# Kernel optimization log

Measured on AMD Instinct MI355X. Metric: run time of the kernel, lower is better.

The kernel has to match this reference:

```python
import jax, jax.numpy as jnp
import numpy as np
from jax import lax

# Fixed LBP neighbor-difference filters: each of 8 filters is (neighbor - center)
_LBP_W = np.array([
    [[[0,0,1],[0,-1,0],[0,0,0]]],
    [[[0,0,0],[0,-1,1],[0,0,0]]],
    [[[0,0,0],[0,-1,0],[0,0,1]]],
    [[[0,0,0],[0,-1,0],[0,1,0]]],
    [[[0,0,0],[0,-1,0],[1,0,0]]],
    [[[0,0,0],[1,-1,0],[0,0,0]]],
    [[[1,0,0],[0,-1,0],[0,0,0]]],
    [[[0,1,0],[0,-1,0],[0,0,0]]],
], dtype=np.float32)  # [8,1,3,3] OIHW

_RGB2GRAY = np.array([0.299, 0.587, 0.114], dtype=np.float32)


def setup_inputs() -> dict:
    key = jax.random.key(0)
    img = jax.random.uniform(key, (16, 3, 1024, 1024), dtype=jnp.float32)
    lbp_weight = jnp.asarray(_LBP_W)                                   # [8,1,3,3]
    kernel_weight = jnp.asarray(2.0 ** np.arange(8, dtype=np.float32)  # 1,2,...,128
                                ).reshape(1, 8, 1, 1)
    return {"img": img, "lbp_weight": lbp_weight, "kernel_weight": kernel_weight}


def reference(img, lbp_weight, kernel_weight):
    # rgb2gray: [B,3,H,W] -> [B,1,H,W]
    gray = jnp.einsum("bchw,c->bhw", img, jnp.asarray(_RGB2GRAY))[:, None]
    # 3x3 LBP neighbor-difference conv, padding=1 (SAME)
    out = lax.conv_general_dilated(
        gray, lbp_weight, window_strides=(1, 1), padding=((1, 1), (1, 1)),
        dimension_numbers=("NCHW", "OIHW", "NCHW"))                    # [B,8,H,W]
    # threshold then weighted sum of bit-planes -> LBP code in [0,255]
    bits = jnp.where(out >= 0.0, 1.0, 0.0)
    lbp_img = jnp.sum(bits * kernel_weight, axis=1)                     # [B,H,W]
    # 256-bin histogram over ALL elements (matches torch.where counting loop)
    idx = lbp_img.astype(jnp.int32).reshape(-1)
    hist = jnp.zeros((1, 256), dtype=jnp.float32).at[0, idx].add(1.0)
    # standardize with unbiased std (torch.std default, ddof=1)
    mean = jnp.mean(hist, axis=1, keepdims=True)
    std = jnp.sqrt(jnp.sum((hist - mean) ** 2, axis=1, keepdims=True) / (256 - 1))
    return (hist - mean) / std
```

## Files before the change

kernel.cpp:

```cpp
#include <hip/hip_runtime.h>

#define NBATCH  16
#define NSTRIPS 16
#define SEGROWS 64
#define NSEGS   (1024 / SEGROWS)
#define NWAVES  (NBATCH * NSEGS * NSTRIPS)
#define NBLOCKS (NWAVES / 4)
#define NHIST   8

__device__ __forceinline__ float gray3(float r, float g, float b) {
    return (r * 0.299f + g * 0.587f) + b * 0.114f;
}

__global__ __launch_bounds__(256) void lbp_hist_kernel(
        const float* __restrict__ img, unsigned* __restrict__ g_hist) {
    __shared__ unsigned s_hist[4][256];
    const int tid  = threadIdx.x;
    const int wv   = tid >> 6;
    const int lane = tid & 63;
    #pragma unroll
    for (int i = 0; i < 4; ++i) s_hist[i][tid] = 0u;
    __syncthreads();

    const int w     = blockIdx.x * 4 + wv;
    const int strip = w & (NSTRIPS - 1);
    const int seg   = (w >> 4) & (NSEGS - 1);
    const int b     = w >> 8;
    const int wx    = strip << 6;
    const int x     = wx + lane;
    const int y0    = seg * SEGROWS;
    const int ylast = y0 + SEGROWS;

    const float* R = img + (size_t)b * 3145728u;
    const float* G = R + 1048576;
    const float* B = R + 2097152;

    const bool hL  = (lane == 0);
    const bool hR  = (lane == 63);
    const int  hx  = hL ? (wx - 1) : (wx + 64);
    const bool hOk = (hL || hR) && ((unsigned)hx < 1024u);

    auto issue = [&](int y, float& rr, float& gg, float& bb,
                     float& hr2, float& hg2, float& hb2) {
        rr = gg = bb = hr2 = hg2 = hb2 = 0.f;
        if ((unsigned)y < 1024u && y <= ylast) {
            const int o = y << 10;
            rr = R[o + x]; gg = G[o + x]; bb = B[o + x];
            if (hOk) { hr2 = R[o + hx]; hg2 = G[o + hx]; hb2 = B[o + hx]; }
        }
    };
    auto finish = [&](float rr, float gg, float bb, float hr2, float hg2, float hb2,
                      float& l, float& c, float& r) {
        const float cc = gray3(rr, gg, bb);
        const float hh = gray3(hr2, hg2, hb2);
        l = __shfl_up(cc, 1);
        r = __shfl_down(cc, 1);
        if (hL) l = hh;
        if (hR) r = hh;
        c = cc;
    };

    float r0l, r0c, r0r, r1l, r1c, r1r, r2l, r2c, r2r;
    float p1r, p1g, p1b, p1hr, p1hg, p1hb;
    float p2r, p2g, p2b, p2hr, p2hg, p2hb;
    float nr,  ng,  nb,  nhr,  nhg,  nhb;

    issue(y0 - 1, p1r, p1g, p1b, p1hr, p1hg, p1hb);
    finish(p1r, p1g, p1b, p1hr, p1hg, p1hb, r0l, r0c, r0r);
    issue(y0,     p1r, p1g, p1b, p1hr, p1hg, p1hb);
    finish(p1r, p1g, p1b, p1hr, p1hg, p1hb, r1l, r1c, r1r);
    issue(y0 + 1, p1r, p1g, p1b, p1hr, p1hg, p1hb);
    issue(y0 + 2, p2r, p2g, p2b, p2hr, p2hg, p2hb);

    unsigned cnt0 = 0u, cnt255 = 0u;

    #pragma unroll 4
    for (int y = y0; y < y0 + SEGROWS; ++y) {
        issue(y + 3, nr, ng, nb, nhr, nhg, nhb);
        finish(p1r, p1g, p1b, p1hr, p1hg, p1hb, r2l, r2c, r2r);

        const unsigned code =
            (r0r >= r1c ?   1u : 0u) |
            (r1r >= r1c ?   2u : 0u) |
            (r2r >= r1c ?   4u : 0u) |
            (r2c >= r1c ?   8u : 0u) |
            (r2l >= r1c ?  16u : 0u) |
            (r1l >= r1c ?  32u : 0u) |
            (r0l >= r1c ?  64u : 0u) |
            (r0c >= r1c ? 128u : 0u);

        cnt0   += (unsigned)__popcll(__ballot(code ==   0u));
        cnt255 += (unsigned)__popcll(__ballot(code == 255u));
        if ((code - 1u) < 254u)
            atomicAdd(&s_hist[wv][code], 1u);

        r0l = r1l; r0c = r1c; r0r = r1r;
        r1l = r2l; r1c = r2c; r1r = r2r;
        p1r = p2r; p1g = p2g; p1b = p2b; p1hr = p2hr; p1hg = p2hg; p1hb = p2hb;
        p2r = nr;  p2g = ng;  p2b = nb;  p2hr = nhr;  p2hg = nhg;  p2hb = nhb;
    }

    if (lane == 0) {
        atomicAdd(&s_hist[wv][0],   cnt0);
        atomicAdd(&s_hist[wv][255], cnt255);
    }
    __syncthreads();
    const unsigned total = s_hist[0][tid] + s_hist[1][tid] + s_hist[2][tid] + s_hist[3][tid];
    atomicAdd(&g_hist[((blockIdx.x & (NHIST - 1)) << 8) + tid], total);
}

__global__ __launch_bounds__(256) void lbp_finalize(
        const unsigned* __restrict__ g_hist, float* __restrict__ out) {
    __shared__ float red[256];
    const int i = threadIdx.x;
    unsigned hv = 0u;
    #pragma unroll
    for (int c = 0; c < NHIST; ++c) hv += g_hist[(c << 8) + i];
    const float h = (float)hv;
    red[i] = h;
    __syncthreads();
    #pragma unroll
    for (int s = 128; s > 0; s >>= 1) {
        if (i < s) red[i] += red[i + s];
        __syncthreads();
    }
    const float mean = red[0] * (1.0f / 256.0f);
    __syncthreads();
    const float d = h - mean;
    red[i] = d * d;
    __syncthreads();
    #pragma unroll
    for (int s = 128; s > 0; s >>= 1) {
        if (i < s) red[i] += red[i + s];
        __syncthreads();
    }
    const float stdv = sqrtf(red[0] * (1.0f / 255.0f));
    out[i] = d / stdv;
}

extern "C" void kernel_launch(void* const* d_in, const int* in_sizes, int n_in,
                              void* d_out, int out_size, void* d_ws, size_t ws_size,
                              hipStream_t stream) {
    const float* img = (const float*)d_in[0];
    unsigned* g_hist = (unsigned*)d_ws;
    float* out = (float*)d_out;

    hipMemsetAsync(g_hist, 0, NHIST * 256 * sizeof(unsigned), stream);
    lbp_hist_kernel<<<NBLOCKS, 256, 0, stream>>>(img, g_hist);
    lbp_finalize<<<1, 256, 0, stream>>>(g_hist, out);
}
```

Baseline: 283.2 us.

## Vectorize loads to float4 per lane and fuse finalize into last block

Each lane now handles four adjacent columns using float4 loads, so a wave covers 256 columns. The segment height is halved to keep enough waves in flight, and launch bounds request two blocks per CU. The separate finalize kernel is folded into the histogram kernel: the last block to finish, found through an atomic counter, performs the standardization. This cuts the number of load instructions and one kernel launch, at the cost of more registers per thread and a threadfence/atomic handshake at the end of every block.

```diff
diff --git a/kernel.cpp b/kernel.cpp
--- a/kernel.cpp
+++ b/kernel.cpp
@@ -1,10 +1,11 @@
 #include <hip/hip_runtime.h>
 
 #define NBATCH  16
-#define NSTRIPS 16
-#define SEGROWS 64
+#define COLS_W  256
+#define NSTRIPS (1024 / COLS_W)
+#define SEGROWS 32
 #define NSEGS   (1024 / SEGROWS)
-#define NWAVES  (NBATCH * NSEGS * NSTRIPS)
+#define NWAVES  (NBATCH * NSTRIPS * NSEGS)
 #define NBLOCKS (NWAVES / 4)
 #define NHIST   8
 
@@ -12,9 +13,12 @@
     return (r * 0.299f + g * 0.587f) + b * 0.114f;
 }
 
-__global__ __launch_bounds__(256) void lbp_hist_kernel(
-        const float* __restrict__ img, unsigned* __restrict__ g_hist) {
+__global__ __launch_bounds__(256, 2) void lbp_hist_kernel(
+        const float* __restrict__ img, unsigned* __restrict__ g_hist,
+        float* __restrict__ out) {
     __shared__ unsigned s_hist[4][256];
+    __shared__ float red[256];
+    __shared__ int s_last;
     const int tid  = threadIdx.x;
     const int wv   = tid >> 6;
     const int lane = tid & 63;
@@ -24,10 +28,10 @@
 
     const int w     = blockIdx.x * 4 + wv;
     const int strip = w & (NSTRIPS - 1);
-    const int seg   = (w >> 4) & (NSEGS - 1);
-    const int b     = w >> 8;
-    const int wx    = strip << 6;
-    const int x     = wx + lane;
+    const int seg   = (w >> 2) & (NSEGS - 1);
+    const int b     = w >> 7;
+    const int wx    = strip * COLS_W;
+    const int x     = wx + 4 * lane;
     const int y0    = seg * SEGROWS;
     const int ylast = y0 + SEGROWS;
 
@@ -37,38 +41,43 @@
 
     const bool hL  = (lane == 0);
     const bool hR  = (lane == 63);
-    const int  hx  = hL ? (wx - 1) : (wx + 64);
+    const int  hx  = hL ? (wx - 1) : (wx + COLS_W);
     const bool hOk = (hL || hR) && ((unsigned)hx < 1024u);
 
-    auto issue = [&](int y, float& rr, float& gg, float& bb,
+    auto issue = [&](int y, float4& rr, float4& gg, float4& bb,
                      float& hr2, float& hg2, float& hb2) {
-        rr = gg = bb = hr2 = hg2 = hb2 = 0.f;
+        rr = gg = bb = make_float4(0.f, 0.f, 0.f, 0.f);
+        hr2 = hg2 = hb2 = 0.f;
         if ((unsigned)y < 1024u && y <= ylast) {
             const int o = y << 10;
-            rr = R[o + x]; gg = G[o + x]; bb = B[o + x];
+            rr = *(const float4*)(R + o + x);
+            gg = *(const float4*)(G + o + x);
+            bb = *(const float4*)(B + o + x);
             if (hOk) { hr2 = R[o + hx]; hg2 = G[o + hx]; hb2 = B[o + hx]; }
         }
     };
-    auto finish = [&](float rr, float gg, float bb, float hr2, float hg2, float hb2,
-                      float& l, float& c, float& r) {
-        const float cc = gray3(rr, gg, bb);
+    auto finish = [&](const float4& rr, const float4& gg, const float4& bb,
+                      float hr2, float hg2, float hb2, float* row) {
+        row[1] = gray3(rr.x, gg.x, bb.x);
+        row[2] = gray3(rr.y, gg.y, bb.y);
+        row[3] = gray3(rr.z, gg.z, bb.z);
+        row[4] = gray3(rr.w, gg.w, bb.w);
         const float hh = gray3(hr2, hg2, hb2);
-        l = __shfl_up(cc, 1);
-        r = __shfl_down(cc, 1);
-        if (hL) l = hh;
-        if (hR) r = hh;
-        c = cc;
+        const float lu = __shfl_up(row[4], 1);
+        const float rd = __shfl_down(row[1], 1);
+        row[0] = hL ? hh : lu;
+        row[5] = hR ? hh : rd;
     };
 
-    float r0l, r0c, r0r, r1l, r1c, r1r, r2l, r2c, r2r;
-    float p1r, p1g, p1b, p1hr, p1hg, p1hb;
-    float p2r, p2g, p2b, p2hr, p2hg, p2hb;
-    float nr,  ng,  nb,  nhr,  nhg,  nhb;
+    float r0[6], r1[6], r2[6];
+    float4 p1r, p1g, p1b;  float p1hr, p1hg, p1hb;
+    float4 p2r, p2g, p2b;  float p2hr, p2hg, p2hb;
+    float4 nr,  ng,  nb;   float nhr,  nhg,  nhb;
 
     issue(y0 - 1, p1r, p1g, p1b, p1hr, p1hg, p1hb);
-    finish(p1r, p1g, p1b, p1hr, p1hg, p1hb, r0l, r0c, r0r);
+    finish(p1r, p1g, p1b, p1hr, p1hg, p1hb, r0);
     issue(y0,     p1r, p1g, p1b, p1hr, p1hg, p1hb);
-    finish(p1r, p1g, p1b, p1hr, p1hg, p1hb, r1l, r1c, r1r);
+    finish(p1r, p1g, p1b, p1hr, p1hg, p1hb, r1);
     issue(y0 + 1, p1r, p1g, p1b, p1hr, p1hg, p1hb);
     issue(y0 + 2, p2r, p2g, p2b, p2hr, p2hg, p2hb);
 
@@ -77,25 +86,28 @@
     #pragma unroll 4
     for (int y = y0; y < y0 + SEGROWS; ++y) {
         issue(y + 3, nr, ng, nb, nhr, nhg, nhb);
-        finish(p1r, p1g, p1b, p1hr, p1hg, p1hb, r2l, r2c, r2r);
+        finish(p1r, p1g, p1b, p1hr, p1hg, p1hb, r2);
 
-        const unsigned code =
-            (r0r >= r1c ?   1u : 0u) |
-            (r1r >= r1c ?   2u : 0u) |
-            (r2r >= r1c ?   4u : 0u) |
-            (r2c >= r1c ?   8u : 0u) |
-            (r2l >= r1c ?  16u : 0u) |
-            (r1l >= r1c ?  32u : 0u) |
-            (r0l >= r1c ?  64u : 0u) |
-            (r0c >= r1c ? 128u : 0u);
+        #pragma unroll
+        for (int k = 0; k < 4; ++k) {
+            const float c = r1[k + 1];
+            const unsigned code =
+                (r0[k + 2] >= c ?   1u : 0u) |
+                (r1[k + 2] >= c ?   2u : 0u) |
+                (r2[k + 2] >= c ?   4u : 0u) |
+                (r2[k + 1] >= c ?   8u : 0u) |
+                (r2[k]     >= c ?  16u : 0u) |
+                (r1[k]     >= c ?  32u : 0u) |
+                (r0[k]     >= c ?  64u : 0u) |
+                (r0[k + 1] >= c ? 128u : 0u);
+            cnt0   += (unsigned)__popcll(__ballot(code ==   0u));
+            cnt255 += (unsigned)__popcll(__ballot(code == 255u));
+            if ((code - 1u) < 254u)
+                atomicAdd(&s_hist[wv][code], 1u);
+        }
 
-        cnt0   += (unsigned)__popcll(__ballot(code ==   0u));
-        cnt255 += (unsigned)__popcll(__ballot(code == 255u));
-        if ((code - 1u) < 254u)
-            atomicAdd(&s_hist[wv][code], 1u);
-
-        r0l = r1l; r0c = r1c; r0r = r1r;
-        r1l = r2l; r1c = r2c; r1r = r2r;
+        #pragma unroll
+        for (int i = 0; i < 6; ++i) { r0[i] = r1[i]; r1[i] = r2[i]; }
         p1r = p2r; p1g = p2g; p1b = p2b; p1hr = p2hr; p1hg = p2hg; p1hb = p2hb;
         p2r = nr;  p2g = ng;  p2b = nb;  p2hr = nhr;  p2hg = nhg;  p2hb = nhb;
     }
@@ -107,35 +119,40 @@
     __syncthreads();
     const unsigned total = s_hist[0][tid] + s_hist[1][tid] + s_hist[2][tid] + s_hist[3][tid];
     atomicAdd(&g_hist[((blockIdx.x & (NHIST - 1)) << 8) + tid], total);
-}
 
-__global__ __launch_bounds__(256) void lbp_finalize(
-        const unsigned* __restrict__ g_hist, float* __restrict__ out) {
-    __shared__ float red[256];
-    const int i = threadIdx.x;
-    unsigned hv = 0u;
-    #pragma unroll
-    for (int c = 0; c < NHIST; ++c) hv += g_hist[(c << 8) + i];
-    const float h = (float)hv;
-    red[i] = h;
+    __threadfence();
+    if (tid == 0) {
+        const unsigned rank = atomicAdd(&g_hist[NHIST * 256], 1u);
+        s_last = (rank == NBLOCKS - 1) ? 1 : 0;
+    }
     __syncthreads();
-    #pragma unroll
-    for (int s = 128; s > 0; s >>= 1) {
-        if (i < s) red[i] += red[i + s];
+    if (s_last) {
+        __threadfence();
+        unsigned hv = 0u;
+        #pragma unroll
+        for (int c2 = 0; c2 < NHIST; ++c2)
+            hv += __hip_atomic_load(&g_hist[(c2 << 8) + tid],
+                                    __ATOMIC_RELAXED, __HIP_MEMORY_SCOPE_AGENT);
+        const float h = (float)hv;
+        red[tid] = h;
         __syncthreads();
+        #pragma unroll
+        for (int s = 128; s > 0; s >>= 1) {
+            if (tid < s) red[tid] += red[tid + s];
+            __syncthreads();
+        }
+        const float mean = red[0] * (1.0f / 256.0f);
+        __syncthreads();
+        const float d = h - mean;
+        red[tid] = d * d;
+        __syncthreads();
+        #pragma unroll
+        for (int s = 128; s > 0; s >>= 1) {
+            if (tid < s) red[tid] += red[tid + s];
+            __syncthreads();
+        }
+        out[tid] = d / sqrtf(red[0] * (1.0f / 255.0f));
     }
-    const float mean = red[0] * (1.0f / 256.0f);
-    __syncthreads();
-    const float d = h - mean;
-    red[i] = d * d;
-    __syncthreads();
-    #pragma unroll
-    for (int s = 128; s > 0; s >>= 1) {
-        if (i < s) red[i] += red[i + s];
-        __syncthreads();
-    }
-    const float stdv = sqrtf(red[0] * (1.0f / 255.0f));
-    out[i] = d / stdv;
 }
 
 extern "C" void kernel_launch(void* const* d_in, const int* in_sizes, int n_in,
@@ -145,7 +162,6 @@
     unsigned* g_hist = (unsigned*)d_ws;
     float* out = (float*)d_out;
 
-    hipMemsetAsync(g_hist, 0, NHIST * 256 * sizeof(unsigned), stream);
-    lbp_hist_kernel<<<NBLOCKS, 256, 0, stream>>>(img, g_hist);
-    lbp_finalize<<<1, 256, 0, stream>>>(g_hist, out);
+    hipMemsetAsync(g_hist, 0, (NHIST * 256 + 4) * sizeof(unsigned), stream);
+    lbp_hist_kernel<<<NBLOCKS, 256, 0, stream>>>(img, g_hist, out);
 }
```

After: 330.5 us. 16.7% more time.
